# Performance work log

Measured on AMD Instinct MI355X. Metric: run time of the kernel, lower is better.

## Reference

```python
import jax, jax.numpy as jnp
import numpy as np

B, N, D = 4, 16384, 128       # batch, tokens (mesh points), input_dim
H, DH = 8, 64                 # heads, dim_head
INNER = H * DH


def setup_inputs() -> dict:
    key = jax.random.key(0)
    ks = jax.random.split(key, 7)
    s = 0.02  # weight init scale
    return {
        "queries": jax.random.normal(ks[0], (B, N, D), jnp.float32),
        "keys":    jax.random.normal(ks[1], (B, N, D), jnp.float32),
        "values":  jax.random.normal(ks[2], (B, N, D), jnp.float32),
        "Wq": jax.random.normal(ks[3], (INNER, D), jnp.float32) * s,
        "Wk": jax.random.normal(ks[4], (INNER, D), jnp.float32) * s,
        "Wo": jax.random.normal(ks[5], (D, INNER), jnp.float32) * s,
        "bo": jnp.zeros((D,), jnp.float32),
    }


def _split_heads(x, b, n):
    # [b, n, h*d] -> [b, h, n, d]
    return x.reshape(b, n, H, DH).transpose(0, 2, 1, 3)


def reference(queries, keys, values, Wq, Wk, Wo, bo):
    b, n, _ = queries.shape
    q = _split_heads(queries @ Wq.T, b, n)
    k = _split_heads(keys    @ Wk.T, b, n)
    # NOTE: original source applies to_k to values (bug kept for faithfulness)
    v = _split_heads(values  @ Wk.T, b, n)
    # Galerkin linear attention, associative order: q @ (k^T v) / n.
    # (In the runnable no-mask path the instance norms are computed but
    #  discarded by the original code, so they are omitted here.)
    dots = jnp.einsum('bhnd,bhne->bhde', k, v)          # [b,h,d,d]
    out = jnp.einsum('bhnd,bhde->bhne', q, dots) / n    # [b,h,n,d]
    out = out.transpose(0, 2, 1, 3).reshape(b, n, INNER)
    return out @ Wo.T + bo
```

## Files before the change

### kernel.cpp

```cpp
#include <hip/hip_runtime.h>
#include <hip/hip_bf16.h>

#define BB    4
#define NN    16384
#define DD    128
#define HH    8
#define DHH   64
#define INNER 512
#define PC    64

typedef __attribute__((ext_vector_type(8))) short bf16x8;
typedef __attribute__((ext_vector_type(4))) float f32x4;
typedef unsigned short ushort_t;

#define MFMA(a, b, c) __builtin_amdgcn_mfma_f32_16x16x32_bf16((a), (b), (c), 0, 0, 0)

__device__ __forceinline__ short f2bf(float x) {
    union { float f; unsigned u; } v; v.f = x;
    unsigned u = v.u;
    u += 0x7fffu + ((u >> 16) & 1u);
    return (short)(u >> 16);
}

__device__ __forceinline__ float bf2f(ushort_t us) {
    union { unsigned u; float f; } v;
    v.u = ((unsigned)us) << 16;
    return v.f;
}

__device__ __forceinline__ bf16x8 load_row8(const float* __restrict__ p) {
    f32x4 a = *(const f32x4*)p;
    f32x4 b = *(const f32x4*)(p + 4);
    bf16x8 r;
    r[0] = f2bf(a[0]); r[1] = f2bf(a[1]); r[2] = f2bf(a[2]); r[3] = f2bf(a[3]);
    r[4] = f2bf(b[0]); r[5] = f2bf(b[1]); r[6] = f2bf(b[2]); r[7] = f2bf(b[3]);
    return r;
}

__device__ __forceinline__ bf16x8 load_col8(const float* __restrict__ p, int stride) {
    bf16x8 r;
#pragma unroll
    for (int j = 0; j < 8; ++j) r[j] = f2bf(p[(size_t)j * stride]);
    return r;
}

__global__ __launch_bounds__(512) void k1_partialS(
        const float* __restrict__ keys, const float* __restrict__ vals,
        ushort_t* __restrict__ partial) {
    const int b     = blockIdx.x >> 6;
    const int chunk = blockIdx.x & (PC - 1);
    const int r0    = chunk * (NN / PC);
    const int lane  = threadIdx.x & 63;
    const int w     = threadIdx.x >> 6;
    const int mw    = w & 3;
    const int nw    = w >> 2;
    const int ml    = lane & 15;
    const int quad  = lane >> 4;

    const float* kbase = keys + (size_t)b * NN * DD;
    const float* vbase = vals + (size_t)b * NN * DD;

    f32x4 acc[2][4];
#pragma unroll
    for (int i = 0; i < 2; ++i)
#pragma unroll
        for (int t = 0; t < 4; ++t) acc[i][t] = (f32x4){0.f, 0.f, 0.f, 0.f};

    for (int n0 = r0; n0 < r0 + (NN / PC); n0 += 32) {
        const int nbase = n0 + quad * 8;
        bf16x8 a[2];
#pragma unroll
        for (int i = 0; i < 2; ++i)
            a[i] = load_col8(kbase + (size_t)nbase * DD + (2 * mw + i) * 16 + ml, DD);
#pragma unroll
        for (int t = 0; t < 4; ++t) {
            const int e = (nw * 4 + t) * 16 + ml;
            bf16x8 bf = load_col8(vbase + (size_t)nbase * DD + e, DD);
            acc[0][t] = MFMA(a[0], bf, acc[0][t]);
            acc[1][t] = MFMA(a[1], bf, acc[1][t]);
        }
    }
    ushort_t* outp = partial + (size_t)blockIdx.x * DD * DD;
#pragma unroll
    for (int i = 0; i < 2; ++i) {
        const int mrow = (2 * mw + i) * 16 + quad * 4;
#pragma unroll
        for (int t = 0; t < 4; ++t) {
            const int col = (nw * 4 + t) * 16 + ml;
#pragma unroll
            for (int r = 0; r < 4; ++r)
                outp[(size_t)(mrow + r) * DD + col] = (ushort_t)f2bf(acc[i][t][r]);
        }
    }
}

__global__ __launch_bounds__(256) void k2_reduce(
        const ushort_t* __restrict__ partial, float* __restrict__ S,
        float* __restrict__ G) {
    const int t   = blockIdx.x * 256 + threadIdx.x;
    const int b   = t >> 14;
    const int idx = t & 16383;
    const ushort_t* p = partial + ((size_t)b * PC) * DD * DD + idx;
    float s = 0.f;
#pragma unroll 16
    for (int c = 0; c < PC; ++c) s += bf2f(p[(size_t)c * DD * DD]);
    S[t] = s;
    G[t] = 0.f;
}

__global__ __launch_bounds__(256) void k3_middle(
        const float* __restrict__ S, const float* __restrict__ Wq,
        const float* __restrict__ Wk, const float* __restrict__ Wo,
        float* __restrict__ G) {
    const int b    = blockIdx.x >> 3;
    const int h    = blockIdx.x & 7;
    const int lane = threadIdx.x & 63;
    const int w    = threadIdx.x >> 6;
    const int ml   = lane & 15;
    const int quad = lane >> 4;

    __shared__ short lds[22528];
    short* T1 = lds;
    short* dT = lds + 8704;
    short* T2 = lds + 13312;

    const float* Sb  = S  + (size_t)b * DD * DD;
    const float* Wkh = Wk + (size_t)h * DHH * DD;
    const float* Wqh = Wq + (size_t)h * DHH * DD;

    {
        f32x4 acc[4][2];
#pragma unroll
        for (int mi = 0; mi < 4; ++mi)
#pragma unroll
            for (int j = 0; j < 2; ++j) acc[mi][j] = (f32x4){0.f, 0.f, 0.f, 0.f};
#pragma unroll
        for (int kc = 0; kc < 4; ++kc) {
            const int c0 = kc * 32 + quad * 8;
            bf16x8 a[4];
#pragma unroll
            for (int mi = 0; mi < 4; ++mi)
                a[mi] = load_row8(Wkh + (size_t)(mi * 16 + ml) * DD + c0);
#pragma unroll
            for (int j = 0; j < 2; ++j) {
                bf16x8 bf = load_col8(Sb + (size_t)c0 * DD + (2 * w + j) * 16 + ml, DD);
#pragma unroll
                for (int mi = 0; mi < 4; ++mi)
                    acc[mi][j] = MFMA(a[mi], bf, acc[mi][j]);
            }
        }
#pragma unroll
        for (int mi = 0; mi < 4; ++mi)
#pragma unroll
            for (int j = 0; j < 2; ++j)
#pragma unroll
                for (int r = 0; r < 4; ++r)
                    T1[(mi * 16 + quad * 4 + r) * 136 + (2 * w + j) * 16 + ml] =
                        f2bf(acc[mi][j][r]);
    }
    __syncthreads();

    {
        f32x4 acc[4];
#pragma unroll
        for (int t = 0; t < 4; ++t) acc[t] = (f32x4){0.f, 0.f, 0.f, 0.f};
#pragma unroll
        for (int kc = 0; kc < 4; ++kc) {
            const int c0 = kc * 32 + quad * 8;
            bf16x8 a = *(const bf16x8*)&T1[(w * 16 + ml) * 136 + c0];
#pragma unroll
            for (int t = 0; t < 4; ++t) {
                bf16x8 bf = load_row8(Wkh + (size_t)(t * 16 + ml) * DD + c0);
                acc[t] = MFMA(a, bf, acc[t]);
            }
        }
#pragma unroll
        for (int t = 0; t < 4; ++t)
#pragma unroll
            for (int r = 0; r < 4; ++r)
                dT[(t * 16 + ml) * 72 + w * 16 + quad * 4 + r] = f2bf(acc[t][r]);
    }
    __syncthreads();

    {
        f32x4 acc[2][4];
#pragma unroll
        for (int i = 0; i < 2; ++i)
#pragma unroll
            for (int t = 0; t < 4; ++t) acc[i][t] = (f32x4){0.f, 0.f, 0.f, 0.f};
#pragma unroll
        for (int kc = 0; kc < 2; ++kc) {
            const int d0 = kc * 32 + quad * 8;
            bf16x8 a[2];
#pragma unroll
            for (int i = 0; i < 2; ++i) {
                const int cp = (2 * w + i) * 16 + ml;
                a[i] = load_col8(Wqh + (size_t)d0 * DD + cp, DD);
            }
#pragma unroll
            for (int t = 0; t < 4; ++t) {
                bf16x8 bf = *(const bf16x8*)&dT[(t * 16 + ml) * 72 + d0];
                acc[0][t] = MFMA(a[0], bf, acc[0][t]);
                acc[1][t] = MFMA(a[1], bf, acc[1][t]);
            }
        }
#pragma unroll
        for (int i = 0; i < 2; ++i)
#pragma unroll
            for (int t = 0; t < 4; ++t)
#pragma unroll
                for (int r = 0; r < 4; ++r)
                    T2[((2 * w + i) * 16 + quad * 4 + r) * 72 + t * 16 + ml] =
                        f2bf(acc[i][t][r]);
    }
    __syncthreads();

    {
        f32x4 acc[2][8];
#pragma unroll
        for (int i = 0; i < 2; ++i)
#pragma unroll
            for (int t = 0; t < 8; ++t) acc[i][t] = (f32x4){0.f, 0.f, 0.f, 0.f};
#pragma unroll
        for (int kc = 0; kc < 2; ++kc) {
            const int e0 = kc * 32 + quad * 8;
            bf16x8 a[2];
#pragma unroll
            for (int i = 0; i < 2; ++i)
                a[i] = *(const bf16x8*)&T2[((2 * w + i) * 16 + ml) * 72 + e0];
#pragma unroll
            for (int t = 0; t < 8; ++t) {
                bf16x8 bf = load_row8(Wo + (size_t)(t * 16 + ml) * INNER + h * DHH + e0);
                acc[0][t] = MFMA(a[0], bf, acc[0][t]);
                acc[1][t] = MFMA(a[1], bf, acc[1][t]);
            }
        }
        float* Gb = G + (size_t)b * DD * DD;
#pragma unroll
        for (int i = 0; i < 2; ++i)
#pragma unroll
            for (int t = 0; t < 8; ++t)
#pragma unroll
                for (int r = 0; r < 4; ++r)
                    atomicAdd(&Gb[((2 * w + i) * 16 + quad * 4 + r) * DD + t * 16 + ml],
                              acc[i][t][r]);
    }
}

__global__ __launch_bounds__(256) void k4_final(
        const float* __restrict__ queries, const float* __restrict__ G,
        const float* __restrict__ bo, float* __restrict__ outp) {
    const int b  = blockIdx.x >> 7;
    const int r0 = (blockIdx.x & 127) * 128;

    __shared__ short Gt[128 * 136];
    {
        const float* Gb = G + (size_t)b * DD * DD;
        const float invN = 6.103515625e-05f;
#pragma unroll 4
        for (int it = 0; it < 64; ++it) {
            const int idx = threadIdx.x + it * 256;
            const int cp = idx >> 7, c = idx & 127;
            Gt[c * 136 + cp] = f2bf(Gb[idx] * invN);
        }
    }
    __syncthreads();

    const int lane = threadIdx.x & 63;
    const int w    = threadIdx.x >> 6;
    const int ml   = lane & 15;
    const int quad = lane >> 4;
    const float* qbase = queries + ((size_t)b * NN + r0) * DD;

    f32x4 acc[2][8];
#pragma unroll
    for (int i = 0; i < 2; ++i)
#pragma unroll
        for (int t = 0; t < 8; ++t) acc[i][t] = (f32x4){0.f, 0.f, 0.f, 0.f};

#pragma unroll
    for (int kc = 0; kc < 4; ++kc) {
        const int k0 = kc * 32 + quad * 8;
        bf16x8 a[2];
#pragma unroll
        for (int i = 0; i < 2; ++i)
            a[i] = load_row8(qbase + (size_t)((2 * w + i) * 16 + ml) * DD + k0);
#pragma unroll
        for (int t = 0; t < 8; ++t) {
            bf16x8 bf = *(const bf16x8*)&Gt[(t * 16 + ml) * 136 + k0];
            acc[0][t] = MFMA(a[0], bf, acc[0][t]);
            acc[1][t] = MFMA(a[1], bf, acc[1][t]);
        }
    }

    float* ob = outp + ((size_t)b * NN + r0) * DD;
#pragma unroll
    for (int t = 0; t < 8; ++t) {
        const int c = t * 16 + ml;
        const float boc = bo[c];
#pragma unroll
        for (int i = 0; i < 2; ++i)
#pragma unroll
            for (int r = 0; r < 4; ++r)
                ob[(size_t)((2 * w + i) * 16 + quad * 4 + r) * DD + c] =
                    acc[i][t][r] + boc;
    }
}

extern "C" void kernel_launch(void* const* d_in, const int* in_sizes, int n_in,
                              void* d_out, int out_size, void* d_ws, size_t ws_size,
                              hipStream_t stream) {
    const float* queries = (const float*)d_in[0];
    const float* keys    = (const float*)d_in[1];
    const float* values  = (const float*)d_in[2];
    const float* Wq      = (const float*)d_in[3];
    const float* Wk      = (const float*)d_in[4];
    const float* Wo      = (const float*)d_in[5];
    const float* bo      = (const float*)d_in[6];
    float* out = (float*)d_out;

    float* S = (float*)d_ws;
    float* G = S + (size_t)BB * DD * DD;
    ushort_t* partial = (ushort_t*)(G + (size_t)BB * DD * DD);

    hipLaunchKernelGGL(k1_partialS, dim3(BB * PC), dim3(512), 0, stream,
                       keys, values, partial);
    hipLaunchKernelGGL(k2_reduce, dim3(256), dim3(256), 0, stream,
                       partial, S, G);
    hipLaunchKernelGGL(k3_middle, dim3(BB * HH), dim3(256), 0, stream,
                       S, Wq, Wk, Wo, G);
    hipLaunchKernelGGL(k4_final, dim3(512), dim3(256), 0, stream,
                       queries, G, bo, out);
}
```

Measured before the change: 178.7 us.

## Precompute per-head weight products to shorten the middle GEMM chain

The k1 kernel gains 16 extra blocks. They compute per-head bf16 products of weight pairs: Wq_h^T·Wk_h, and Wo_h·Wk_h for the output side. The middle kernel then does two 128x128 GEMMs against S instead of a four-stage dependent chain with three barriers, which cuts its latency and its strided weight loads. The final kernel also moves to 512-thread blocks covering 256 rows each, halving the number of G staging passes. The risk is that the fused weight products add bf16 rounding and make each GEMM in the small k3 grid larger.

```diff
diff --git a/kernel.cpp b/kernel.cpp
--- a/kernel.cpp
+++ b/kernel.cpp
@@ -44,52 +44,106 @@
     return r;
 }
 
-__global__ __launch_bounds__(512) void k1_partialS(
+__global__ __launch_bounds__(512) void k1_partialS_ab(
         const float* __restrict__ keys, const float* __restrict__ vals,
-        ushort_t* __restrict__ partial) {
-    const int b     = blockIdx.x >> 6;
-    const int chunk = blockIdx.x & (PC - 1);
-    const int r0    = chunk * (NN / PC);
-    const int lane  = threadIdx.x & 63;
-    const int w     = threadIdx.x >> 6;
-    const int mw    = w & 3;
-    const int nw    = w >> 2;
-    const int ml    = lane & 15;
-    const int quad  = lane >> 4;
-
-    const float* kbase = keys + (size_t)b * NN * DD;
-    const float* vbase = vals + (size_t)b * NN * DD;
-
-    f32x4 acc[2][4];
-#pragma unroll
-    for (int i = 0; i < 2; ++i)
-#pragma unroll
-        for (int t = 0; t < 4; ++t) acc[i][t] = (f32x4){0.f, 0.f, 0.f, 0.f};
-
-    for (int n0 = r0; n0 < r0 + (NN / PC); n0 += 32) {
-        const int nbase = n0 + quad * 8;
-        bf16x8 a[2];
-#pragma unroll
-        for (int i = 0; i < 2; ++i)
-            a[i] = load_col8(kbase + (size_t)nbase * DD + (2 * mw + i) * 16 + ml, DD);
-#pragma unroll
-        for (int t = 0; t < 4; ++t) {
-            const int e = (nw * 4 + t) * 16 + ml;
-            bf16x8 bf = load_col8(vbase + (size_t)nbase * DD + e, DD);
-            acc[0][t] = MFMA(a[0], bf, acc[0][t]);
-            acc[1][t] = MFMA(a[1], bf, acc[1][t]);
-        }
-    }
-    ushort_t* outp = partial + (size_t)blockIdx.x * DD * DD;
-#pragma unroll
-    for (int i = 0; i < 2; ++i) {
-        const int mrow = (2 * mw + i) * 16 + quad * 4;
-#pragma unroll
-        for (int t = 0; t < 4; ++t) {
-            const int col = (nw * 4 + t) * 16 + ml;
-#pragma unroll
-            for (int r = 0; r < 4; ++r)
-                outp[(size_t)(mrow + r) * DD + col] = (ushort_t)f2bf(acc[i][t][r]);
+        const float* __restrict__ Wq, const float* __restrict__ Wk,
+        const float* __restrict__ Wo,
+        ushort_t* __restrict__ partial, ushort_t* __restrict__ Abf,
+        ushort_t* __restrict__ BTbf) {
+    const int lane = threadIdx.x & 63;
+    const int w    = threadIdx.x >> 6;
+    const int ml   = lane & 15;
+    const int quad = lane >> 4;
+
+    if (blockIdx.x < BB * PC) {
+        const int b     = blockIdx.x >> 6;
+        const int chunk = blockIdx.x & (PC - 1);
+        const int r0    = chunk * (NN / PC);
+        const int mw    = w & 3;
+        const int nw    = w >> 2;
+
+        const float* kbase = keys + (size_t)b * NN * DD;
+        const float* vbase = vals + (size_t)b * NN * DD;
+
+        f32x4 acc[2][4];
+#pragma unroll
+        for (int i = 0; i < 2; ++i)
+#pragma unroll
+            for (int t = 0; t < 4; ++t) acc[i][t] = (f32x4){0.f, 0.f, 0.f, 0.f};
+
+        for (int n0 = r0; n0 < r0 + (NN / PC); n0 += 32) {
+            const int nbase = n0 + quad * 8;
+            bf16x8 a[2];
+#pragma unroll
+            for (int i = 0; i < 2; ++i)
+                a[i] = load_col8(kbase + (size_t)nbase * DD + (2 * mw + i) * 16 + ml, DD);
+#pragma unroll
+            for (int t = 0; t < 4; ++t) {
+                const int e = (nw * 4 + t) * 16 + ml;
+                bf16x8 bf = load_col8(vbase + (size_t)nbase * DD + e, DD);
+                acc[0][t] = MFMA(a[0], bf, acc[0][t]);
+                acc[1][t] = MFMA(a[1], bf, acc[1][t]);
+            }
+        }
+        ushort_t* outp = partial + (size_t)blockIdx.x * DD * DD;
+#pragma unroll
+        for (int i = 0; i < 2; ++i) {
+            const int mrow = (2 * mw + i) * 16 + quad * 4;
+#pragma unroll
+            for (int t = 0; t < 4; ++t) {
+                const int col = (nw * 4 + t) * 16 + ml;
+#pragma unroll
+                for (int r = 0; r < 4; ++r)
+                    outp[(size_t)(mrow + r) * DD + col] = (ushort_t)f2bf(acc[i][t][r]);
+            }
+        }
+    } else {
+        const int ab    = blockIdx.x - BB * PC;
+        const int h     = ab & 7;
+        const int which = ab >> 3;
+        const float* Wkh = Wk + (size_t)h * DHH * DD;
+
+        f32x4 acc[8];
+#pragma unroll
+        for (int t = 0; t < 8; ++t) acc[t] = (f32x4){0.f, 0.f, 0.f, 0.f};
+
+        if (which == 0) {
+            const float* Wqh = Wq + (size_t)h * DHH * DD;
+#pragma unroll
+            for (int kc = 0; kc < 2; ++kc) {
+                const int d0 = kc * 32 + quad * 8;
+                bf16x8 a = load_col8(Wqh + (size_t)d0 * DD + w * 16 + ml, DD);
+#pragma unroll
+                for (int t = 0; t < 8; ++t) {
+                    bf16x8 bf = load_col8(Wkh + (size_t)d0 * DD + t * 16 + ml, DD);
+                    acc[t] = MFMA(a, bf, acc[t]);
+                }
+            }
+            ushort_t* dst = Abf + (size_t)h * DD * DD;
+#pragma unroll
+            for (int t = 0; t < 8; ++t)
+#pragma unroll
+                for (int r = 0; r < 4; ++r)
+                    dst[(size_t)(w * 16 + quad * 4 + r) * DD + t * 16 + ml] =
+                        (ushort_t)f2bf(acc[t][r]);
+        } else {
+#pragma unroll
+            for (int kc = 0; kc < 2; ++kc) {
+                const int e0 = kc * 32 + quad * 8;
+                bf16x8 a = load_row8(Wo + (size_t)(w * 16 + ml) * INNER + h * DHH + e0);
+#pragma unroll
+                for (int t = 0; t < 8; ++t) {
+                    bf16x8 bf = load_col8(Wkh + (size_t)e0 * DD + t * 16 + ml, DD);
+                    acc[t] = MFMA(a, bf, acc[t]);
+                }
+            }
+            ushort_t* dst = BTbf + (size_t)h * DD * DD;
+#pragma unroll
+            for (int t = 0; t < 8; ++t)
+#pragma unroll
+                for (int r = 0; r < 4; ++r)
+                    dst[(size_t)(w * 16 + quad * 4 + r) * DD + t * 16 + ml] =
+                        (ushort_t)f2bf(acc[t][r]);
         }
     }
 }
@@ -109,9 +163,8 @@
 }
 
 __global__ __launch_bounds__(256) void k3_middle(
-        const float* __restrict__ S, const float* __restrict__ Wq,
-        const float* __restrict__ Wk, const float* __restrict__ Wo,
-        float* __restrict__ G) {
+        const float* __restrict__ S, const ushort_t* __restrict__ Abf,
+        const ushort_t* __restrict__ BTbf, float* __restrict__ G) {
     const int b    = blockIdx.x >> 3;
     const int h    = blockIdx.x & 7;
     const int lane = threadIdx.x & 63;
@@ -119,87 +172,28 @@
     const int ml   = lane & 15;
     const int quad = lane >> 4;
 
-    __shared__ short lds[22528];
-    short* T1 = lds;
-    short* dT = lds + 8704;
-    short* T2 = lds + 13312;
-
-    const float* Sb  = S  + (size_t)b * DD * DD;
-    const float* Wkh = Wk + (size_t)h * DHH * DD;
-    const float* Wqh = Wq + (size_t)h * DHH * DD;
+    __shared__ short T[128 * 136];
+
+    const float*    Sb = S    + (size_t)b * DD * DD;
+    const ushort_t* Ah = Abf  + (size_t)h * DD * DD;
+    const ushort_t* Bh = BTbf + (size_t)h * DD * DD;
 
     {
-        f32x4 acc[4][2];
-#pragma unroll
-        for (int mi = 0; mi < 4; ++mi)
-#pragma unroll
-            for (int j = 0; j < 2; ++j) acc[mi][j] = (f32x4){0.f, 0.f, 0.f, 0.f};
+        f32x4 acc[2][8];
+#pragma unroll
+        for (int i = 0; i < 2; ++i)
+#pragma unroll
+            for (int t = 0; t < 8; ++t) acc[i][t] = (f32x4){0.f, 0.f, 0.f, 0.f};
 #pragma unroll
         for (int kc = 0; kc < 4; ++kc) {
             const int c0 = kc * 32 + quad * 8;
-            bf16x8 a[4];
-#pragma unroll
-            for (int mi = 0; mi < 4; ++mi)
-                a[mi] = load_row8(Wkh + (size_t)(mi * 16 + ml) * DD + c0);
-#pragma unroll
-            for (int j = 0; j < 2; ++j) {
-                bf16x8 bf = load_col8(Sb + (size_t)c0 * DD + (2 * w + j) * 16 + ml, DD);
-#pragma unroll
-                for (int mi = 0; mi < 4; ++mi)
-                    acc[mi][j] = MFMA(a[mi], bf, acc[mi][j]);
-            }
-        }
-#pragma unroll
-        for (int mi = 0; mi < 4; ++mi)
-#pragma unroll
-            for (int j = 0; j < 2; ++j)
-#pragma unroll
-                for (int r = 0; r < 4; ++r)
-                    T1[(mi * 16 + quad * 4 + r) * 136 + (2 * w + j) * 16 + ml] =
-                        f2bf(acc[mi][j][r]);
-    }
-    __syncthreads();
-
-    {
-        f32x4 acc[4];
-#pragma unroll
-        for (int t = 0; t < 4; ++t) acc[t] = (f32x4){0.f, 0.f, 0.f, 0.f};
-#pragma unroll
-        for (int kc = 0; kc < 4; ++kc) {
-            const int c0 = kc * 32 + quad * 8;
-            bf16x8 a = *(const bf16x8*)&T1[(w * 16 + ml) * 136 + c0];
-#pragma unroll
-            for (int t = 0; t < 4; ++t) {
-                bf16x8 bf = load_row8(Wkh + (size_t)(t * 16 + ml) * DD + c0);
-                acc[t] = MFMA(a, bf, acc[t]);
-            }
-        }
-#pragma unroll
-        for (int t = 0; t < 4; ++t)
-#pragma unroll
-            for (int r = 0; r < 4; ++r)
-                dT[(t * 16 + ml) * 72 + w * 16 + quad * 4 + r] = f2bf(acc[t][r]);
-    }
-    __syncthreads();
-
-    {
-        f32x4 acc[2][4];
-#pragma unroll
-        for (int i = 0; i < 2; ++i)
-#pragma unroll
-            for (int t = 0; t < 4; ++t) acc[i][t] = (f32x4){0.f, 0.f, 0.f, 0.f};
-#pragma unroll
-        for (int kc = 0; kc < 2; ++kc) {
-            const int d0 = kc * 32 + quad * 8;
             bf16x8 a[2];
 #pragma unroll
-            for (int i = 0; i < 2; ++i) {
-                const int cp = (2 * w + i) * 16 + ml;
-                a[i] = load_col8(Wqh + (size_t)d0 * DD + cp, DD);
-            }
-#pragma unroll
-            for (int t = 0; t < 4; ++t) {
-                bf16x8 bf = *(const bf16x8*)&dT[(t * 16 + ml) * 72 + d0];
+            for (int i = 0; i < 2; ++i)
+                a[i] = *(const bf16x8*)&Ah[(size_t)((2 * w + i) * 16 + ml) * DD + c0];
+#pragma unroll
+            for (int t = 0; t < 8; ++t) {
+                bf16x8 bf = load_col8(Sb + (size_t)c0 * DD + t * 16 + ml, DD);
                 acc[0][t] = MFMA(a[0], bf, acc[0][t]);
                 acc[1][t] = MFMA(a[1], bf, acc[1][t]);
             }
@@ -207,10 +201,10 @@
 #pragma unroll
         for (int i = 0; i < 2; ++i)
 #pragma unroll
-            for (int t = 0; t < 4; ++t)
-#pragma unroll
-                for (int r = 0; r < 4; ++r)
-                    T2[((2 * w + i) * 16 + quad * 4 + r) * 72 + t * 16 + ml] =
+            for (int t = 0; t < 8; ++t)
+#pragma unroll
+                for (int r = 0; r < 4; ++r)
+                    T[((2 * w + i) * 16 + quad * 4 + r) * 136 + t * 16 + ml] =
                         f2bf(acc[i][t][r]);
     }
     __syncthreads();
@@ -222,15 +216,15 @@
 #pragma unroll
             for (int t = 0; t < 8; ++t) acc[i][t] = (f32x4){0.f, 0.f, 0.f, 0.f};
 #pragma unroll
-        for (int kc = 0; kc < 2; ++kc) {
-            const int e0 = kc * 32 + quad * 8;
+        for (int kc = 0; kc < 4; ++kc) {
+            const int k0 = kc * 32 + quad * 8;
             bf16x8 a[2];
 #pragma unroll
             for (int i = 0; i < 2; ++i)
-                a[i] = *(const bf16x8*)&T2[((2 * w + i) * 16 + ml) * 72 + e0];
+                a[i] = *(const bf16x8*)&T[((2 * w + i) * 16 + ml) * 136 + k0];
 #pragma unroll
             for (int t = 0; t < 8; ++t) {
-                bf16x8 bf = load_row8(Wo + (size_t)(t * 16 + ml) * INNER + h * DHH + e0);
+                bf16x8 bf = *(const bf16x8*)&Bh[(size_t)(t * 16 + ml) * DD + k0];
                 acc[0][t] = MFMA(a[0], bf, acc[0][t]);
                 acc[1][t] = MFMA(a[1], bf, acc[1][t]);
             }
@@ -247,19 +241,19 @@
     }
 }
 
-__global__ __launch_bounds__(256) void k4_final(
+__global__ __launch_bounds__(512) void k4_final(
         const float* __restrict__ queries, const float* __restrict__ G,
         const float* __restrict__ bo, float* __restrict__ outp) {
-    const int b  = blockIdx.x >> 7;
-    const int r0 = (blockIdx.x & 127) * 128;
+    const int b  = blockIdx.x >> 6;
+    const int r0 = (blockIdx.x & 63) * 256;
 
     __shared__ short Gt[128 * 136];
     {
         const float* Gb = G + (size_t)b * DD * DD;
         const float invN = 6.103515625e-05f;
 #pragma unroll 4
-        for (int it = 0; it < 64; ++it) {
-            const int idx = threadIdx.x + it * 256;
+        for (int it = 0; it < 32; ++it) {
+            const int idx = threadIdx.x + it * 512;
             const int cp = idx >> 7, c = idx & 127;
             Gt[c * 136 + cp] = f2bf(Gb[idx] * invN);
         }
@@ -321,14 +315,16 @@
 
     float* S = (float*)d_ws;
     float* G = S + (size_t)BB * DD * DD;
-    ushort_t* partial = (ushort_t*)(G + (size_t)BB * DD * DD);
-
-    hipLaunchKernelGGL(k1_partialS, dim3(BB * PC), dim3(512), 0, stream,
-                       keys, values, partial);
+    ushort_t* Abf     = (ushort_t*)(G + (size_t)BB * DD * DD);
+    ushort_t* BTbf    = Abf  + (size_t)HH * DD * DD;
+    ushort_t* partial = BTbf + (size_t)HH * DD * DD;
+
+    hipLaunchKernelGGL(k1_partialS_ab, dim3(BB * PC + 16), dim3(512), 0, stream,
+                       keys, values, Wq, Wk, Wo, partial, Abf, BTbf);
     hipLaunchKernelGGL(k2_reduce, dim3(256), dim3(256), 0, stream,
                        partial, S, G);
     hipLaunchKernelGGL(k3_middle, dim3(BB * HH), dim3(256), 0, stream,
-                       S, Wq, Wk, Wo, G);
-    hipLaunchKernelGGL(k4_final, dim3(512), dim3(256), 0, stream,
+                       S, Abf, BTbf, G);
+    hipLaunchKernelGGL(k4_final, dim3(256), dim3(512), 0, stream,
                        queries, G, bo, out);
 }
```

Result: no change. 177.0 us (-0.9%).
